# Optimization experiments

Measured on AMD Instinct MI355X. Metric: run time of the kernel, lower is better.

Reference implementation:

```python
import jax, jax.numpy as jnp
import numpy as np

INPUT_CHANNELS = 6
RESERVOIR_SIZE = 256
SPECTRAL_RADIUS = 0.9
SPARSITY = 0.8
BATCH = 256
SEQ_LEN = 512


def _make_reservoir_weights(seed=0):
    rng = np.random.RandomState(seed)
    W_res = rng.randn(RESERVOIR_SIZE, RESERVOIR_SIZE).astype(np.float32)
    mask = (rng.rand(RESERVOIR_SIZE, RESERVOIR_SIZE) > SPARSITY).astype(np.float32)
    W_res = W_res * mask
    cur_radius = np.abs(np.linalg.eigvals(W_res)).max()
    if cur_radius > 0:
        W_res = W_res * (SPECTRAL_RADIUS / cur_radius)
    return W_res.astype(np.float32)


def setup_inputs() -> dict:
    key = jax.random.key(0)
    k_x, k_in = jax.random.split(key)
    x = jax.random.normal(k_x, (BATCH, SEQ_LEN, INPUT_CHANNELS), dtype=jnp.float32)
    W_in = jax.random.normal(k_in, (INPUT_CHANNELS, RESERVOIR_SIZE), dtype=jnp.float32) * 0.1
    W_res = jnp.asarray(_make_reservoir_weights())
    return {"x": x, "W_in": W_in, "W_res": W_res}


def reference(x, W_in, W_res):
    # x: [B, T, C] -> x_proj: [B, T, R]
    x_proj = jnp.einsum("btc,cr->btr", x, W_in)
    B = x.shape[0]
    R = W_res.shape[0]
    h0 = jnp.zeros((B, R), dtype=x.dtype)

    def step(h, xp_t):
        # xp_t: [B, R]
        h_new = jnp.tanh(xp_t + h @ W_res)
        return h_new, h_new

    # scan over time: xs must be time-major [T, B, R]
    _, h_seq = jax.lax.scan(step, h0, jnp.swapaxes(x_proj, 0, 1))
    return jnp.swapaxes(h_seq, 0, 1)  # [B, T, R]
```

## Files before the change

### kernel.cpp

```cpp
#include <hip/hip_runtime.h>

#define BATCH 256
#define SEQ_T 512
#define CIN   6
#define RES   256

__global__ __launch_bounds__(1024, 1)
void esn_scan_kernel(const float* __restrict__ x,
                     const float* __restrict__ W_in,
                     const float* __restrict__ W_res,
                     float* __restrict__ out) {
    __shared__ float h[2][RES];
    __shared__ float part[8][RES];

    const int tid = threadIdx.x;
    const int b   = blockIdx.x;
    const int r   = tid & 127;
    const int kk  = tid >> 7;

    float w0[32], w1[32];
    #pragma unroll
    for (int j = 0; j < 32; ++j) {
        w0[j] = W_res[(kk * 32 + j) * RES + r];
        w1[j] = W_res[(kk * 32 + j) * RES + r + 128];
    }

    float win[CIN];
    if (tid < RES) {
        #pragma unroll
        for (int c = 0; c < CIN; ++c) win[c] = W_in[c * RES + tid];
    }

    if (tid < RES) h[0][tid] = 0.0f;
    __syncthreads();

    const float* xb = x + (size_t)b * SEQ_T * CIN;
    float*       ob = out + (size_t)b * SEQ_T * RES;

    int p = 0;
    for (int t = 0; t < SEQ_T; ++t) {
        float xv[CIN];
        #pragma unroll
        for (int c = 0; c < CIN; ++c) xv[c] = xb[t * CIN + c];

        const float4* hb = (const float4*)(&h[p][kk * 32]);
        float a0 = 0.0f, a1 = 0.0f;
        #pragma unroll
        for (int j = 0; j < 8; ++j) {
            float4 hv = hb[j];
            a0 = fmaf(hv.x, w0[4*j+0], a0); a1 = fmaf(hv.x, w1[4*j+0], a1);
            a0 = fmaf(hv.y, w0[4*j+1], a0); a1 = fmaf(hv.y, w1[4*j+1], a1);
            a0 = fmaf(hv.z, w0[4*j+2], a0); a1 = fmaf(hv.z, w1[4*j+2], a1);
            a0 = fmaf(hv.w, w0[4*j+3], a0); a1 = fmaf(hv.w, w1[4*j+3], a1);
        }
        part[kk][r]       = a0;
        part[kk][r + 128] = a1;
        __syncthreads();

        if (tid < RES) {
            float s = 0.0f;
            #pragma unroll
            for (int c = 0; c < CIN; ++c) s = fmaf(xv[c], win[c], s);
            #pragma unroll
            for (int q = 0; q < 8; ++q) s += part[q][tid];
            float e  = __expf(2.0f * s);
            float hn = 1.0f - 2.0f * __builtin_amdgcn_rcpf(e + 1.0f);
            h[1 - p][tid]   = hn;
            ob[t * RES + tid] = hn;
        }
        __syncthreads();
        p ^= 1;
    }
}

extern "C" void kernel_launch(void* const* d_in, const int* in_sizes, int n_in,
                              void* d_out, int out_size, void* d_ws, size_t ws_size,
                              hipStream_t stream) {
    const float* x     = (const float*)d_in[0];
    const float* W_in  = (const float*)d_in[1];
    const float* W_res = (const float*)d_in[2];
    float*       out   = (float*)d_out;

    esn_scan_kernel<<<BATCH, 1024, 0, stream>>>(x, W_in, W_res, out);
}
```

Before: 479.8 us.

## Reduce recurrent matvec partial sums with DPP across quads, one barrier per step

Each group of four lanes now splits the 256-long dot product for one output neuron, and the partial sums are combined with DPP cross-lane moves instead of a shared-memory partial buffer. This removes one of the two block barriers per timestep and the shared partial-sum traffic. The hidden-state buffer is padded to avoid LDS bank conflicts. A raw s_barrier with a manual lgkmcnt wait replaces __syncthreads, and the time loop is unrolled by two to drop the ping-pong index.

```diff
diff --git a/kernel.cpp b/kernel.cpp
--- a/kernel.cpp
+++ b/kernel.cpp
@@ -4,73 +4,89 @@
 #define SEQ_T 512
 #define CIN   6
 #define RES   256
+#define HPAD  272
+
+template <int CTRL>
+__device__ __forceinline__ float quad_xor_add(float v) {
+    union { float f; int i; } u;
+    u.f = v;
+    u.i = __builtin_amdgcn_mov_dpp(u.i, CTRL, 0xF, 0xF, true);
+    return v + u.f;
+}
 
 __global__ __launch_bounds__(1024, 1)
 void esn_scan_kernel(const float* __restrict__ x,
                      const float* __restrict__ W_in,
                      const float* __restrict__ W_res,
                      float* __restrict__ out) {
-    __shared__ float h[2][RES];
-    __shared__ float part[8][RES];
+    __shared__ float h[2][HPAD];
 
-    const int tid = threadIdx.x;
-    const int b   = blockIdx.x;
-    const int r   = tid & 127;
-    const int kk  = tid >> 7;
+    const int tid  = threadIdx.x;
+    const int b    = blockIdx.x;
+    const int lane = tid & 63;
+    const int wid  = tid >> 6;
+    const int sub  = lane & 3;
+    const int rr   = lane >> 2;
+    const int r    = (wid << 4) | rr;
 
-    float w0[32], w1[32];
+    float w[64];
     #pragma unroll
-    for (int j = 0; j < 32; ++j) {
-        w0[j] = W_res[(kk * 32 + j) * RES + r];
-        w1[j] = W_res[(kk * 32 + j) * RES + r + 128];
-    }
+    for (int j = 0; j < 64; ++j)
+        w[j] = W_res[(sub * 64 + j) * RES + r];
 
     float win[CIN];
-    if (tid < RES) {
-        #pragma unroll
-        for (int c = 0; c < CIN; ++c) win[c] = W_in[c * RES + tid];
-    }
+    #pragma unroll
+    for (int c = 0; c < CIN; ++c) win[c] = W_in[c * RES + r];
 
-    if (tid < RES) h[0][tid] = 0.0f;
+    if (tid < RES) h[0][tid + ((tid >> 6) << 2)] = 0.0f;
     __syncthreads();
 
     const float* xb = x + (size_t)b * SEQ_T * CIN;
-    float*       ob = out + (size_t)b * SEQ_T * RES;
+    float*       ob = out + (size_t)b * SEQ_T * RES + r;
 
-    int p = 0;
-    for (int t = 0; t < SEQ_T; ++t) {
-        float xv[CIN];
-        #pragma unroll
-        for (int c = 0; c < CIN; ++c) xv[c] = xb[t * CIN + c];
+    const int wr = r + ((r >> 6) << 2);
+    const float4* hA = (const float4*)&h[0][sub * 68];
+    const float4* hB = (const float4*)&h[1][sub * 68];
+    float* hAw = &h[0][wr];
+    float* hBw = &h[1][wr];
 
-        const float4* hb = (const float4*)(&h[p][kk * 32]);
-        float a0 = 0.0f, a1 = 0.0f;
-        #pragma unroll
-        for (int j = 0; j < 8; ++j) {
-            float4 hv = hb[j];
-            a0 = fmaf(hv.x, w0[4*j+0], a0); a1 = fmaf(hv.x, w1[4*j+0], a1);
-            a0 = fmaf(hv.y, w0[4*j+1], a0); a1 = fmaf(hv.y, w1[4*j+1], a1);
-            a0 = fmaf(hv.z, w0[4*j+2], a0); a1 = fmaf(hv.z, w1[4*j+2], a1);
-            a0 = fmaf(hv.w, w0[4*j+3], a0); a1 = fmaf(hv.w, w1[4*j+3], a1);
-        }
-        part[kk][r]       = a0;
-        part[kk][r + 128] = a1;
-        __syncthreads();
+#define ESN_STEP(HRD, HWR)                                              \
+    {                                                                   \
+        float xv[CIN];                                                  \
+        _Pragma("unroll")                                               \
+        for (int c = 0; c < CIN; ++c) xv[c] = xb[c];                    \
+        xb += CIN;                                                      \
+        float a0 = 0.f, a1 = 0.f, a2 = 0.f, a3 = 0.f;                   \
+        _Pragma("unroll")                                               \
+        for (int j = 0; j < 16; ++j) {                                  \
+            float4 hv = (HRD)[j];                                       \
+            a0 = fmaf(hv.x, w[4*j+0], a0);                              \
+            a1 = fmaf(hv.y, w[4*j+1], a1);                              \
+            a2 = fmaf(hv.z, w[4*j+2], a2);                              \
+            a3 = fmaf(hv.w, w[4*j+3], a3);                              \
+        }                                                               \
+        float s = (a0 + a1) + (a2 + a3);                                \
+        s = quad_xor_add<0xB1>(s);                        \
+        s = quad_xor_add<0x4E>(s);                        \
+        if (sub == 0) {                                                 \
+            _Pragma("unroll")                                           \
+            for (int c = 0; c < CIN; ++c) s = fmaf(xv[c], win[c], s);   \
+            float e  = __expf(2.0f * s);                                \
+            float hn = 1.0f - 2.0f * __builtin_amdgcn_rcpf(e + 1.0f);   \
+            *(HWR) = hn;                                                \
+            *ob = hn;                                                   \
+        }                                                               \
+        ob += RES;                                                      \
+        asm volatile("s_waitcnt lgkmcnt(0)" ::: "memory");              \
+        __builtin_amdgcn_s_barrier();                                   \
+        asm volatile("" ::: "memory");                                  \
+    }
 
-        if (tid < RES) {
-            float s = 0.0f;
-            #pragma unroll
-            for (int c = 0; c < CIN; ++c) s = fmaf(xv[c], win[c], s);
-            #pragma unroll
-            for (int q = 0; q < 8; ++q) s += part[q][tid];
-            float e  = __expf(2.0f * s);
-            float hn = 1.0f - 2.0f * __builtin_amdgcn_rcpf(e + 1.0f);
-            h[1 - p][tid]   = hn;
-            ob[t * RES + tid] = hn;
-        }
-        __syncthreads();
-        p ^= 1;
+    for (int t = 0; t < SEQ_T; t += 2) {
+        ESN_STEP(hA, hBw);
+        ESN_STEP(hB, hAw);
     }
+#undef ESN_STEP
 }
 
 extern "C" void kernel_launch(void* const* d_in, const int* in_sizes, int n_in,
```

New measurement: 523.4 us. 9.1% more time.
